# Kernel optimization log

Measured on AMD Instinct MI355X. Metric: run time of the kernel, lower is better.

Reference implementation:

```python
import jax, jax.numpy as jnp
import numpy as np

C = 256  # in_channels
B, N = 8, 2048


def setup_inputs() -> dict:
    key = jax.random.key(0)
    ks = jax.random.split(key, 9)
    s = 1.0 / np.sqrt(C)  # conv1d default init scale (approx)
    return {
        "x": jax.random.normal(ks[0], (B, C, N), jnp.float32),
        "wq": jax.random.normal(ks[1], (C, C), jnp.float32) * s,
        "bq": jax.random.normal(ks[2], (C,), jnp.float32) * s,
        "wk": jax.random.normal(ks[3], (C, C), jnp.float32) * s,
        "bk": jax.random.normal(ks[4], (C,), jnp.float32) * s,
        "wv": jax.random.normal(ks[5], (C, C), jnp.float32) * s,
        "bv": jax.random.normal(ks[6], (C,), jnp.float32) * s,
        "wo": jax.random.normal(ks[7], (C, C), jnp.float32) * s,
        "bo": jax.random.normal(ks[8], (C,), jnp.float32) * s,
    }


def reference(x, wq, bq, wk, bk, wv, bv, wo, bo):
    # 1x1 Conv1d == channel-wise linear: [C_out,C_in] x [B,C_in,N] -> [B,C_out,N]
    proj = lambda w, b, t: jnp.einsum('ci,bin->bcn', w, t) + b[None, :, None]
    q = proj(wq, bq, x)
    k = proj(wk, bk, x)
    v = proj(wv, bv, x)
    norm = 1.0 / (x.shape[1] ** 0.5)
    # scores: w[b,n,m] = sum_c q[b,c,n] k[b,c,m]
    w = jnp.einsum('bcn,bcm->bnm', q, k) * norm
    w = jax.nn.softmax(w, axis=2)
    # attn output: sum_m v[b,c,m] w[b,n,m] -> [B,C,N]
    av = jnp.einsum('bcm,bnm->bcn', v, w)
    out = proj(wo, bo, av)
    return x + out
```

## Files before the change

kernel.cpp:

```cpp
#include <hip/hip_runtime.h>
#include <hip/hip_bf16.h>

#define CCH 256
#define NSEQ 2048
#define BATCH 8

typedef __hip_bfloat16 bf16;
typedef short s8v __attribute__((ext_vector_type(8)));
typedef float f4v __attribute__((ext_vector_type(4)));
typedef float f16v __attribute__((ext_vector_type(16)));

struct __align__(8) bf16x4 { bf16 v[4]; };

__device__ __forceinline__ float b2f(bf16 h) { return __bfloat162float(h); }
__device__ __forceinline__ bf16 f2b(float f) { return __float2bfloat16(f); }

#define MFMA16(a, b, c) __builtin_amdgcn_mfma_f32_16x16x32_bf16((a), (b), (c), 0, 0, 0)
#define MFMA32(a, b, c) __builtin_amdgcn_mfma_f32_32x32x16_bf16((a), (b), (c), 0, 0, 0)

__device__ __forceinline__ void gload_lds16(const bf16* g, bf16* l) {
    __builtin_amdgcn_global_load_lds(
        (const __attribute__((address_space(1))) unsigned int*)(g),
        (__attribute__((address_space(3))) unsigned int*)(l), 16, 0, 0);
}

__global__ __launch_bounds__(256) void prepw_kernel(
    const float* __restrict__ wq, const float* __restrict__ wk,
    const float* __restrict__ wv,
    bf16* __restrict__ wqb, bf16* __restrict__ wkb, bf16* __restrict__ wvb)
{
    int base = (blockIdx.x * 256 + threadIdx.x) * 8;
    int mat = base >> 16, off = base & 65535;
    const float* s = (mat == 0) ? wq : (mat == 1) ? wk : wv;
    bf16* d       = (mat == 0) ? wqb : (mat == 1) ? wkb : wvb;
    int doff = off ^ (((off >> 8) & 7) << 3);
    bf16 tmp[8];
    #pragma unroll
    for (int j = 0; j < 8; ++j) tmp[j] = f2b(s[off + j]);
    *(s8v*)&d[doff] = *(const s8v*)tmp;
}

__global__ __launch_bounds__(512, 4) void qkvprep_kernel(
    const float* __restrict__ x,
    const bf16* __restrict__ Wq, const bf16* __restrict__ Wk,
    const bf16* __restrict__ Wv,
    const float* __restrict__ bq, const float* __restrict__ bk,
    const float* __restrict__ bv,
    bf16* __restrict__ qTt, bf16* __restrict__ kTt, bf16* __restrict__ Vt)
{
    __shared__ bf16 xs[64][260];
    __shared__ bf16 wbuf[2][2][4096];

    const int tile = blockIdx.x;
    const int flat0 = tile * 64;
    const int phase = blockIdx.y;
    const int b = flat0 >> 11, nn = flat0 & 2047;
    const int tid = threadIdx.x;
    const int w = tid >> 6, lane = tid & 63;
    const int l15 = lane & 15, quad = lane >> 4;
    const int ng = w & 3;
    const int ch = w >> 2;
    const float* xb = x + (size_t)b * CCH * NSEQ;

    bf16* qt = qTt + (size_t)tile * 16384;
    bf16* kt = kTt + (size_t)tile * 16384;
    bf16* Vtb = Vt + (size_t)b * CCH * NSEQ;

    auto chunk_ptr = [&](int j) -> const bf16* {
        if (phase == 0)
            return (j < 8) ? Wq + (size_t)(ch * 8 + j) * 4096
                           : Wk + (size_t)(ch * 4 + (j - 8)) * 4096;
        else
            return (j < 8) ? Wv + (size_t)(ch * 8 + j) * 4096
                           : Wk + (size_t)(8 + ch * 4 + (j - 8)) * 4096;
    };
    auto stage = [&](int j, int par) {
        const bf16* src = chunk_ptr(j);
        bf16* dst = &wbuf[ch][par][0];
        int seg = (w & 3) * 2;
        gload_lds16(src + (seg + 0) * 512 + lane * 8, dst + (seg + 0) * 512);
        gload_lds16(src + (seg + 1) * 512 + lane * 8, dst + (seg + 1) * 512);
    };

    stage(0, 0);
    #pragma unroll
    for (int i = 0; i < 8; ++i) {
        int f4i = i * 512 + tid;
        int c = f4i >> 4, nq = f4i & 15;
        float4 v4 = *(const float4*)&xb[(size_t)c * NSEQ + nn + nq * 4];
        xs[nq * 4 + 0][c] = f2b(v4.x);
        xs[nq * 4 + 1][c] = f2b(v4.y);
        xs[nq * 4 + 2][c] = f2b(v4.z);
        xs[nq * 4 + 3][c] = f2b(v4.w);
    }
    __syncthreads();

    s8v xf[8];
    #pragma unroll
    for (int t = 0; t < 8; ++t)
        xf[t] = *(const s8v*)&xs[ng * 16 + l15][t * 32 + quad * 8];

    int par = 0;
    #pragma unroll
    for (int j = 0; j < 12; ++j) {
        if (j < 11) stage(j + 1, par ^ 1);

        const char* wb = (const char*)&wbuf[ch][par][0];
        s8v wf[8];
        #pragma unroll
        for (int t = 0; t < 8; ++t)
            wf[t] = *(const s8v*)(wb + l15 * 512 +
                                  ((t * 64 + quad * 16) ^ ((l15 & 7) << 4)));

        if (phase == 0 || j >= 8) {
            f4v a0 = {}, a1 = {};
            #pragma unroll
            for (int t = 0; t < 4; ++t) {
                a0 = MFMA16(wf[t], xf[t], a0);
                a1 = MFMA16(wf[t + 4], xf[t + 4], a1);
            }
            const bool isq = (phase == 0) && (j < 8);
            const int cs = (phase == 0)
                ? (j < 8 ? ch * 8 + j : ch * 4 + (j - 8))
                : (8 + ch * 4 + (j - 8));
            const float* bm = isq ? bq : bk;
            bf16* ot = isq ? qt : kt;
            const float sc = isq ? 0.0625f : 1.0f;
            float4 bb4 = *(const float4*)&bm[cs * 16 + quad * 4];
            float bbr[4] = { bb4.x, bb4.y, bb4.z, bb4.w };
            bf16x4 pk;
            #pragma unroll
            for (int r = 0; r < 4; ++r)
                pk.v[r] = f2b((a0[r] + a1[r] + bbr[r]) * sc);
            int nl = ng * 16 + l15;
            *(bf16x4*)&ot[(cs * 2 + (quad >> 1)) * 512 + nl * 8 + (quad & 1) * 4] = pk;
        } else {
            f4v a0 = {}, a1 = {};
            #pragma unroll
            for (int t = 0; t < 4; ++t) {
                a0 = MFMA16(xf[t], wf[t], a0);
                a1 = MFMA16(xf[t + 4], wf[t + 4], a1);
            }
            const int cs = ch * 8 + j;
            int c = cs * 16 + l15;
            float bb = bv[c];
            bf16x4 pk;
            #pragma unroll
            for (int r = 0; r < 4; ++r)
                pk.v[r] = f2b(a0[r] + a1[r] + bb);
            const int m16 = (nn >> 4) + ng;
            size_t e0 = ((size_t)m16 * 256 + c) * 16 + (quad >> 1) * 8 + (quad & 1) * 4;
            *(bf16x4*)&Vtb[e0] = pk;
        }
        __syncthreads();
        par ^= 1;
    }
}

__global__ __launch_bounds__(256, 2) void flash_kernel(
    const bf16* __restrict__ qTt, const bf16* __restrict__ kTt,
    const bf16* __restrict__ Vt, bf16* __restrict__ Opart,
    float* __restrict__ lpart)
{
    __shared__ bf16 Kc[2][16384];
    __shared__ bf16 Ps[64][68];
    __shared__ float l_s[2][64];

    const int b = blockIdx.x, nt = blockIdx.y, ms = blockIdx.z;
    const int tid = threadIdx.x;
    const int W = tid >> 6, lane = tid & 63;
    const int l31 = lane & 31, h = lane >> 5;
    const int ng = W >> 1, mg = W & 1;
    const int mb = ms * 16;
    const bf16* Vtb = Vt + (size_t)b * CCH * NSEQ;

    s8v qf[16];
    {
        const bf16* qt = qTt + (size_t)(b * 32 + nt) * 16384;
        #pragma unroll
        for (int t = 0; t < 16; ++t)
            qf[t] = *(const s8v*)&qt[(t * 2 + h) * 512 + (ng * 32 + l31) * 8];
    }
    const bf16* vbase = Vtb + (size_t)(W * 64 + l31) * 16 + h * 8;

    f16v O[2][2] = {};
    float lacc[16] = {};

    auto stageK = [&](int a, int buf) {
        const bf16* kt = kTt + (size_t)(b * 32 + a) * 16384;
        #pragma unroll
        for (int i = 0; i < 8; ++i) {
            int ch = W * 8 + i;
            gload_lds16(kt + ch * 512 + lane * 8, &Kc[buf][ch * 512]);
        }
    };

    stageK(mb, 0);
    __syncthreads();

    for (int mt = 0; mt < 16; ++mt) {
        const int cur = mt & 1;
        if (mt < 15) stageK(mb + mt + 1, cur ^ 1);

        f16v S0 = {}, S1 = {};
        __builtin_amdgcn_s_setprio(1);
        #pragma unroll
        for (int t = 0; t < 8; ++t) {
            s8v kf0 = *(const s8v*)&Kc[cur][(t * 2 + h) * 512 + (mg * 32 + l31) * 8];
            s8v kf1 = *(const s8v*)&Kc[cur][((t + 8) * 2 + h) * 512 + (mg * 32 + l31) * 8];
            S0 = MFMA32(qf[t], kf0, S0);
            S1 = MFMA32(qf[t + 8], kf1, S1);
        }
        __builtin_amdgcn_s_setprio(0);
        s8v vf[2][4];
        #pragma unroll
        for (int ks = 0; ks < 4; ++ks)
            #pragma unroll
            for (int cr = 0; cr < 2; ++cr)
                vf[cr][ks] = *(const s8v*)(vbase
                    + (size_t)((mb + mt) * 4 + ks) * 4096 + cr * 512);
        #pragma unroll
        for (int reg = 0; reg < 16; ++reg) {
            float e = __expf(fminf(S0[reg] + S1[reg], 60.f));
            lacc[reg] += e;
            int row = (reg & 3) + 8 * (reg >> 2) + 4 * h;
            Ps[ng * 32 + row][mg * 32 + l31] = f2b(e);
        }
        __syncthreads();

        __builtin_amdgcn_s_setprio(1);
        #pragma unroll
        for (int ks = 0; ks < 4; ++ks) {
            s8v pf0 = *(const s8v*)&Ps[l31][ks * 16 + h * 8];
            s8v pf1 = *(const s8v*)&Ps[32 + l31][ks * 16 + h * 8];
            O[0][0] = MFMA32(vf[0][ks], pf0, O[0][0]);
            O[0][1] = MFMA32(vf[0][ks], pf1, O[0][1]);
            O[1][0] = MFMA32(vf[1][ks], pf0, O[1][0]);
            O[1][1] = MFMA32(vf[1][ks], pf1, O[1][1]);
        }
        __builtin_amdgcn_s_setprio(0);
        __syncthreads();
    }

    #pragma unroll
    for (int reg = 0; reg < 16; ++reg) {
        float s = lacc[reg];
        #pragma unroll
        for (int off = 1; off < 32; off <<= 1) s += __shfl_xor(s, off);
        lacc[reg] = s;
    }
    if (l31 == 0) {
        #pragma unroll
        for (int reg = 0; reg < 16; ++reg) {
            int row = (reg & 3) + 8 * (reg >> 2) + 4 * h;
            l_s[mg][ng * 32 + row] = lacc[reg];
        }
    }
    __syncthreads();
    const size_t pb = (size_t)(b * 32 + nt) * 2 + ms;
    if (tid < 64) lpart[pb * 64 + tid] = l_s[0][tid] + l_s[1][tid];

    bf16* Ob = Opart + pb * 16384;
    #pragma unroll
    for (int cr = 0; cr < 2; ++cr)
        #pragma unroll
        for (int g2 = 0; g2 < 2; ++g2) {
            int n = g2 * 32 + l31;
            #pragma unroll
            for (int q2 = 0; q2 < 4; ++q2) {
                bf16x4 pk;
                #pragma unroll
                for (int j = 0; j < 4; ++j) pk.v[j] = f2b(O[cr][g2][q2 * 4 + j]);
                int c = W * 64 + cr * 32 + q2 * 8 + 4 * h;
                *(bf16x4*)&Ob[(size_t)n * 256 + c] = pk;
            }
        }
}

__global__ __launch_bounds__(256, 2) void outproj_kernel(
    const bf16* __restrict__ Opart, const float* __restrict__ lpart,
    const float* __restrict__ Wo, const float* __restrict__ bo,
    const float* __restrict__ x, float* __restrict__ out)
{
    __shared__ bf16 avs[64][260];
    __shared__ float ils[64];

    const int bx = blockIdx.x;
    const int flat0 = bx * 64;
    const int c0 = blockIdx.y * 128;
    const int tid = threadIdx.x;
    const int w = tid >> 6, lane = tid & 63;
    const int l15 = lane & 15, quad = lane >> 4;

    if (tid < 64)
        ils[tid] = 1.f / (lpart[(size_t)(bx * 2) * 64 + tid]
                        + lpart[(size_t)(bx * 2 + 1) * 64 + tid]);
    __syncthreads();

    const bf16x4* O0 = (const bf16x4*)(Opart + (size_t)(bx * 2) * 16384);
    const bf16x4* O1 = O0 + 4096;
    #pragma unroll
    for (int i = 0; i < 16; ++i) {
        int u = i * 256 + tid;
        int n = u >> 6;
        bf16x4 a = O0[u], bb = O1[u];
        float il = ils[n];
        bf16x4 o;
        #pragma unroll
        for (int t = 0; t < 4; ++t)
            o.v[t] = f2b((b2f(a.v[t]) + b2f(bb.v[t])) * il);
        *(bf16x4*)&avs[n][(u & 63) * 4] = o;
    }
    __syncthreads();

    const int bidx = flat0 >> 11, nn = flat0 & 2047;
    const size_t base = (size_t)bidx * CCH * NSEQ;

    for (int g = 0; g < 2; ++g) {
        const int cg = c0 + g * 64 + w * 16;
        s8v af[8];
        #pragma unroll
        for (int t = 0; t < 8; ++t) {
            const float* wp = Wo + (size_t)(cg + l15) * CCH + t * 32 + quad * 8;
            float4 f0 = *(const float4*)wp;
            float4 f1 = *(const float4*)(wp + 4);
            bf16 a8[8] = { f2b(f0.x), f2b(f0.y), f2b(f0.z), f2b(f0.w),
                           f2b(f1.x), f2b(f1.y), f2b(f1.z), f2b(f1.w) };
            af[t] = *(const s8v*)a8;
        }
        f4v O[4] = {};
        #pragma unroll
        for (int nt = 0; nt < 4; ++nt)
            #pragma unroll
            for (int t = 0; t < 8; ++t) {
                s8v br = *(const s8v*)&avs[nt * 16 + l15][t * 32 + quad * 8];
                O[nt] = MFMA16(af[t], br, O[nt]);
            }
        #pragma unroll
        for (int r = 0; r < 4; ++r) {
            int c = cg + quad * 4 + r;
            float bb = bo[c];
            #pragma unroll
            for (int nt = 0; nt < 4; ++nt) {
                size_t idx = base + (size_t)c * NSEQ + nn + nt * 16 + l15;
                out[idx] = O[nt][r] + bb + x[idx];
            }
        }
    }
}

extern "C" void kernel_launch(void* const* d_in, const int* in_sizes, int n_in,
                              void* d_out, int out_size, void* d_ws, size_t ws_size,
                              hipStream_t stream) {
    (void)in_sizes; (void)n_in; (void)out_size; (void)ws_size;
    const float* x  = (const float*)d_in[0];
    const float* wq = (const float*)d_in[1];
    const float* bq = (const float*)d_in[2];
    const float* wk = (const float*)d_in[3];
    const float* bk = (const float*)d_in[4];
    const float* wv = (const float*)d_in[5];
    const float* bv = (const float*)d_in[6];
    const float* wo = (const float*)d_in[7];
    const float* bo = (const float*)d_in[8];
    float* out = (float*)d_out;

    const size_t T = (size_t)BATCH * CCH * NSEQ;
    bf16* qTt  = (bf16*)d_ws;
    bf16* kTt  = qTt + T;
    bf16* Vt   = kTt + T;
    bf16* wqb  = Vt + T;
    bf16* wkb  = wqb + 65536;
    bf16* wvb  = wkb + 65536;
    float* lpart = (float*)(wvb + 65536);
    bf16* Opart  = (bf16*)(lpart + 32768);

    prepw_kernel<<<96, 256, 0, stream>>>(wq, wk, wv, wqb, wkb, wvb);
    qkvprep_kernel<<<dim3(256, 2), 512, 0, stream>>>(
        x, wqb, wkb, wvb, bq, bk, bv, qTt, kTt, Vt);
    flash_kernel<<<dim3(8, 32, 2), 256, 0, stream>>>(qTt, kTt, Vt, Opart, lpart);
    outproj_kernel<<<dim3(256, 2), 256, 0, stream>>>(Opart, lpart, wo, bo, x, out);
}
```

Measured before the change: 163.5 us.

## Single-buffer K in flash, swap MFMA operands, precast Wo, widen outproj blocks

The flash kernel drops the double-buffered K tile in LDS. The next K tile is now staged after the P-writing barrier, overlapping with the PV MFMAs, which halves K LDS use and may allow higher occupancy. The QK MFMA operand order is swapped so each lane holds one row's scores, which allows vectorized P stores and a single-register row-sum with one shuffle. Wo is converted to bf16 once in the prep kernel, and outproj runs 512-thread blocks with one channel group per wave instead of looping. The trade-off is less prefetch slack for the K load and more threads per outproj block.

After: 155.0 us, median of 3. 5.2% less time.

```diff
diff --git a/kernel.cpp b/kernel.cpp
--- a/kernel.cpp
+++ b/kernel.cpp
@@ -26,14 +26,15 @@
 
 __global__ __launch_bounds__(256) void prepw_kernel(
     const float* __restrict__ wq, const float* __restrict__ wk,
-    const float* __restrict__ wv,
-    bf16* __restrict__ wqb, bf16* __restrict__ wkb, bf16* __restrict__ wvb)
+    const float* __restrict__ wv, const float* __restrict__ wo,
+    bf16* __restrict__ wqb, bf16* __restrict__ wkb,
+    bf16* __restrict__ wvb, bf16* __restrict__ wob)
 {
     int base = (blockIdx.x * 256 + threadIdx.x) * 8;
     int mat = base >> 16, off = base & 65535;
-    const float* s = (mat == 0) ? wq : (mat == 1) ? wk : wv;
-    bf16* d       = (mat == 0) ? wqb : (mat == 1) ? wkb : wvb;
-    int doff = off ^ (((off >> 8) & 7) << 3);
+    const float* s = (mat == 0) ? wq : (mat == 1) ? wk : (mat == 2) ? wv : wo;
+    bf16* d = (mat == 0) ? wqb : (mat == 1) ? wkb : (mat == 2) ? wvb : wob;
+    int doff = (mat == 3) ? off : (off ^ (((off >> 8) & 7) << 3));
     bf16 tmp[8];
     #pragma unroll
     for (int j = 0; j < 8; ++j) tmp[j] = f2b(s[off + j]);
@@ -162,7 +163,7 @@
     const bf16* __restrict__ Vt, bf16* __restrict__ Opart,
     float* __restrict__ lpart)
 {
-    __shared__ bf16 Kc[2][16384];
+    __shared__ bf16 Kc[16384];
     __shared__ bf16 Ps[64][68];
     __shared__ float l_s[2][64];
 
@@ -184,32 +185,29 @@
     const bf16* vbase = Vtb + (size_t)(W * 64 + l31) * 16 + h * 8;
 
     f16v O[2][2] = {};
-    float lacc[16] = {};
-
-    auto stageK = [&](int a, int buf) {
+    float lsum = 0.f;
+
+    auto stageK = [&](int a) {
         const bf16* kt = kTt + (size_t)(b * 32 + a) * 16384;
         #pragma unroll
         for (int i = 0; i < 8; ++i) {
             int ch = W * 8 + i;
-            gload_lds16(kt + ch * 512 + lane * 8, &Kc[buf][ch * 512]);
+            gload_lds16(kt + ch * 512 + lane * 8, &Kc[ch * 512]);
         }
     };
 
-    stageK(mb, 0);
+    stageK(mb);
     __syncthreads();
 
     for (int mt = 0; mt < 16; ++mt) {
-        const int cur = mt & 1;
-        if (mt < 15) stageK(mb + mt + 1, cur ^ 1);
-
         f16v S0 = {}, S1 = {};
         __builtin_amdgcn_s_setprio(1);
         #pragma unroll
         for (int t = 0; t < 8; ++t) {
-            s8v kf0 = *(const s8v*)&Kc[cur][(t * 2 + h) * 512 + (mg * 32 + l31) * 8];
-            s8v kf1 = *(const s8v*)&Kc[cur][((t + 8) * 2 + h) * 512 + (mg * 32 + l31) * 8];
-            S0 = MFMA32(qf[t], kf0, S0);
-            S1 = MFMA32(qf[t + 8], kf1, S1);
+            s8v kf0 = *(const s8v*)&Kc[(t * 2 + h) * 512 + (mg * 32 + l31) * 8];
+            s8v kf1 = *(const s8v*)&Kc[((t + 8) * 2 + h) * 512 + (mg * 32 + l31) * 8];
+            S0 = MFMA32(kf0, qf[t], S0);
+            S1 = MFMA32(kf1, qf[t + 8], S1);
         }
         __builtin_amdgcn_s_setprio(0);
         s8v vf[2][4];
@@ -220,13 +218,19 @@
                 vf[cr][ks] = *(const s8v*)(vbase
                     + (size_t)((mb + mt) * 4 + ks) * 4096 + cr * 512);
         #pragma unroll
-        for (int reg = 0; reg < 16; ++reg) {
-            float e = __expf(fminf(S0[reg] + S1[reg], 60.f));
-            lacc[reg] += e;
-            int row = (reg & 3) + 8 * (reg >> 2) + 4 * h;
-            Ps[ng * 32 + row][mg * 32 + l31] = f2b(e);
+        for (int q = 0; q < 4; ++q) {
+            bf16x4 pk;
+            #pragma unroll
+            for (int r = 0; r < 4; ++r) {
+                float e = __expf(fminf(S0[q * 4 + r] + S1[q * 4 + r], 60.f));
+                lsum += e;
+                pk.v[r] = f2b(e);
+            }
+            *(bf16x4*)&Ps[ng * 32 + l31][mg * 32 + q * 8 + h * 4] = pk;
         }
         __syncthreads();
+
+        if (mt < 15) stageK(mb + mt + 1);
 
         __builtin_amdgcn_s_setprio(1);
         #pragma unroll
@@ -242,19 +246,9 @@
         __syncthreads();
     }
 
-    #pragma unroll
-    for (int reg = 0; reg < 16; ++reg) {
-        float s = lacc[reg];
-        #pragma unroll
-        for (int off = 1; off < 32; off <<= 1) s += __shfl_xor(s, off);
-        lacc[reg] = s;
-    }
-    if (l31 == 0) {
-        #pragma unroll
-        for (int reg = 0; reg < 16; ++reg) {
-            int row = (reg & 3) + 8 * (reg >> 2) + 4 * h;
-            l_s[mg][ng * 32 + row] = lacc[reg];
-        }
+    {
+        float s = lsum + __shfl_xor(lsum, 32);
+        if (h == 0) l_s[mg][ng * 32 + l31] = s;
     }
     __syncthreads();
     const size_t pb = (size_t)(b * 32 + nt) * 2 + ms;
@@ -277,9 +271,9 @@
         }
 }
 
-__global__ __launch_bounds__(256, 2) void outproj_kernel(
+__global__ __launch_bounds__(512, 4) void outproj_kernel(
     const bf16* __restrict__ Opart, const float* __restrict__ lpart,
-    const float* __restrict__ Wo, const float* __restrict__ bo,
+    const bf16* __restrict__ Wob, const float* __restrict__ bo,
     const float* __restrict__ x, float* __restrict__ out)
 {
     __shared__ bf16 avs[64][260];
@@ -300,8 +294,8 @@
     const bf16x4* O0 = (const bf16x4*)(Opart + (size_t)(bx * 2) * 16384);
     const bf16x4* O1 = O0 + 4096;
     #pragma unroll
-    for (int i = 0; i < 16; ++i) {
-        int u = i * 256 + tid;
+    for (int i = 0; i < 8; ++i) {
+        int u = i * 512 + tid;
         int n = u >> 6;
         bf16x4 a = O0[u], bb = O1[u];
         float il = ils[n];
@@ -315,36 +309,29 @@
 
     const int bidx = flat0 >> 11, nn = flat0 & 2047;
     const size_t base = (size_t)bidx * CCH * NSEQ;
-
-    for (int g = 0; g < 2; ++g) {
-        const int cg = c0 + g * 64 + w * 16;
-        s8v af[8];
+    const int cg = c0 + w * 16;
+
+    s8v af[8];
+    #pragma unroll
+    for (int t = 0; t < 8; ++t)
+        af[t] = *(const s8v*)&Wob[(size_t)(cg + l15) * CCH + t * 32 + quad * 8];
+
+    f4v O[4] = {};
+    #pragma unroll
+    for (int nt = 0; nt < 4; ++nt)
         #pragma unroll
         for (int t = 0; t < 8; ++t) {
-            const float* wp = Wo + (size_t)(cg + l15) * CCH + t * 32 + quad * 8;
-            float4 f0 = *(const float4*)wp;
-            float4 f1 = *(const float4*)(wp + 4);
-            bf16 a8[8] = { f2b(f0.x), f2b(f0.y), f2b(f0.z), f2b(f0.w),
-                           f2b(f1.x), f2b(f1.y), f2b(f1.z), f2b(f1.w) };
-            af[t] = *(const s8v*)a8;
-        }
-        f4v O[4] = {};
-        #pragma unroll
-        for (int nt = 0; nt < 4; ++nt)
-            #pragma unroll
-            for (int t = 0; t < 8; ++t) {
-                s8v br = *(const s8v*)&avs[nt * 16 + l15][t * 32 + quad * 8];
-                O[nt] = MFMA16(af[t], br, O[nt]);
-            }
-        #pragma unroll
-        for (int r = 0; r < 4; ++r) {
-            int c = cg + quad * 4 + r;
-            float bb = bo[c];
-            #pragma unroll
-            for (int nt = 0; nt < 4; ++nt) {
-                size_t idx = base + (size_t)c * NSEQ + nn + nt * 16 + l15;
-                out[idx] = O[nt][r] + bb + x[idx];
-            }
+            s8v br = *(const s8v*)&avs[nt * 16 + l15][t * 32 + quad * 8];
+            O[nt] = MFMA16(af[t], br, O[nt]);
+        }
+    #pragma unroll
+    for (int r = 0; r < 4; ++r) {
+        int c = cg + quad * 4 + r;
+        float bb = bo[c];
+        #pragma unroll
+        for (int nt = 0; nt < 4; ++nt) {
+            size_t idx = base + (size_t)c * NSEQ + nn + nt * 16 + l15;
+            out[idx] = O[nt][r] + bb + x[idx];
         }
     }
 }
@@ -371,12 +358,13 @@
     bf16* wqb  = Vt + T;
     bf16* wkb  = wqb + 65536;
     bf16* wvb  = wkb + 65536;
-    float* lpart = (float*)(wvb + 65536);
+    bf16* wob  = wvb + 65536;
+    float* lpart = (float*)(wob + 65536);
     bf16* Opart  = (bf16*)(lpart + 32768);
 
-    prepw_kernel<<<96, 256, 0, stream>>>(wq, wk, wv, wqb, wkb, wvb);
+    prepw_kernel<<<128, 256, 0, stream>>>(wq, wk, wv, wo, wqb, wkb, wvb, wob);
     qkvprep_kernel<<<dim3(256, 2), 512, 0, stream>>>(
         x, wqb, wkb, wvb, bq, bk, bv, qTt, kTt, Vt);
     flash_kernel<<<dim3(8, 32, 2), 256, 0, stream>>>(qTt, kTt, Vt, Opart, lpart);
-    outproj_kernel<<<dim3(256, 2), 256, 0, stream>>>(Opart, lpart, wo, bo, x, out);
-}
+    outproj_kernel<<<dim3(256, 2), 512, 0, stream>>>(Opart, lpart, wob, bo, x, out);
+}
```
